# Kernel optimization log

Hardware: AMD Instinct MI355X
Metric: run time of the kernel (lower is better)

Reference implementation:

```python
import jax, jax.numpy as jnp
import numpy as np

BN_EPS = 1e-5


def three_nn(unknown, known):
    # unknown: (B,n,3), known: (B,m,3) -> dist (B,n,3), idx (B,n,3)
    d2 = (jnp.sum(unknown**2, -1)[:, :, None]
          + jnp.sum(known**2, -1)[:, None, :]
          - 2.0 * jnp.einsum('bnd,bmd->bnm', unknown, known))
    neg_d2, idx = jax.lax.top_k(-d2, 3)  # 3 smallest squared distances
    dist = jnp.sqrt(jnp.maximum(-neg_d2, 0.0))
    return dist, idx


def three_interpolate(points, idx, weight):
    # points: (B,m,c), idx: (B,n,3), weight: (B,n,3) -> (B,n,c)
    gathered = jax.vmap(lambda f, i: f[i])(points, idx)  # (B,n,3,c)
    return jnp.einsum('bnk,bnkc->bnc', weight, gathered)


def conv_bn_relu(x, W, b, g, beta):
    # 1x1 conv over points == per-point linear; BN over (batch, points)
    y = jnp.einsum('bnc,oc->bno', x, W) + b
    mu = jnp.mean(y, axis=(0, 1))
    var = jnp.var(y, axis=(0, 1))
    y = (y - mu) * jax.lax.rsqrt(var + BN_EPS) * g + beta
    return jax.nn.relu(y)


def setup_inputs() -> dict:
    key = jax.random.key(0)
    ks = jax.random.split(key, 8)
    B, n, m, C1, C2 = 8, 8192, 2048, 128, 256
    Cin = C1 + C2  # 384
    H = 256
    return {
        'unknown': jax.random.normal(ks[0], (B, n, 3), jnp.float32),
        'known': jax.random.normal(ks[1], (B, m, 3), jnp.float32),
        'unknow_feats': jax.random.normal(ks[2], (B, n, C1), jnp.float32),
        'known_feats': jax.random.normal(ks[3], (B, m, C2), jnp.float32),
        'W1': jax.random.normal(ks[4], (H, Cin), jnp.float32) * (1.0 / np.sqrt(Cin)),
        'b1': jnp.zeros((H,), jnp.float32),
        'g1': jnp.ones((H,), jnp.float32),
        'beta1': jnp.zeros((H,), jnp.float32),
        'W2': jax.random.normal(ks[5], (H, H), jnp.float32) * (1.0 / np.sqrt(H)),
        'b2': jnp.zeros((H,), jnp.float32),
        'g2': jnp.ones((H,), jnp.float32),
        'beta2': jnp.zeros((H,), jnp.float32),
    }


def reference(unknown, known, unknow_feats, known_feats,
              W1, b1, g1, beta1, W2, b2, g2, beta2):
    dist, idx = three_nn(unknown, known)
    dist = dist + 1e-10
    dist_recip = 1.0 / dist
    weight = dist_recip / jnp.sum(dist_recip, axis=2, keepdims=True)  # (B,n,3)
    interpolated = three_interpolate(known_feats, idx, weight)        # (B,n,C2)
    new_points = jnp.concatenate([interpolated, unknow_feats], axis=-1)  # (B,n,C1+C2)
    new_points = conv_bn_relu(new_points, W1, b1, g1, beta1)
    new_points = conv_bn_relu(new_points, W2, b2, g2, beta2)
    return new_points  # (B,n,mlp[-1])
```

## Files before the change

kernel.cpp:

```cpp
#include <hip/hip_runtime.h>

#define BQ   8
#define NQ   8192
#define MK   2048
#define C1v  128
#define C2v  256
#define CIN  384
#define HH   256
#define MTOT (BQ*NQ)

#define NCHUNK 8
#define CHSZ   (MK/NCHUNK)

typedef __attribute__((ext_vector_type(8))) __bf16 bf16x8;
typedef __attribute__((ext_vector_type(4))) float f32x4;
typedef __attribute__((ext_vector_type(8))) unsigned short us8;
typedef __attribute__((ext_vector_type(4))) unsigned short us4;
typedef __attribute__((ext_vector_type(2))) unsigned short us2;

__device__ __forceinline__ unsigned short f2bf(float f) {
  unsigned int u = __builtin_bit_cast(unsigned int, f);
  u += 0x7fffu + ((u >> 16) & 1u);
  return (unsigned short)(u >> 16);
}
__device__ __forceinline__ float bf2f(unsigned short h) {
  unsigned int u = ((unsigned int)h) << 16;
  return __builtin_bit_cast(float, u);
}

__device__ __forceinline__ void gload16(const void* g, void* l) {
  __builtin_amdgcn_global_load_lds((const __attribute__((address_space(1))) void*)g,
                                   (__attribute__((address_space(3))) void*)l, 16, 0, 0);
}

__device__ __forceinline__ unsigned int cvtpk_bf16(float lo, float hi) {
  unsigned int r;
  asm("v_cvt_pk_bf16_f32 %0, %1, %2" : "=v"(r) : "v"(lo), "v"(hi));
  return r;
}

#define SCORE(k4) (fmaf((k4).x, ux, fmaf((k4).y, uy, (k4).z * uz)) + (k4).w)

__device__ __forceinline__ double packsd(float s, int negj) {
  unsigned long long u = __builtin_bit_cast(unsigned long long, (double)s)
                       | (unsigned long long)(unsigned int)negj;
  return __builtin_bit_cast(double, u);
}

#define INS3D(s0, s1, s2, t)                                  \
  do {                                                        \
    double _hi0 = fmax(s0, (t)), _lo0 = fmin(s0, (t));        \
    double _hi1 = fmax(s1, _lo0), _lo1 = fmin(s1, _lo0);      \
    s0 = _hi0; s1 = _hi1; s2 = fmax(s2, _lo1);                \
  } while (0)

__global__ __launch_bounds__(256)
void prep_kernel(const float* __restrict__ W1, const float* __restrict__ W2,
                 const float* __restrict__ known,
                 unsigned short* __restrict__ w1b, unsigned short* __restrict__ w2b,
                 float* __restrict__ stats, float4* __restrict__ kprep) {
  int i = blockIdx.x * 256 + threadIdx.x;
  if (i < HH*CIN) w1b[i] = f2bf(W1[i]);
  else if (i < HH*CIN + HH*HH) w2b[i - HH*CIN] = f2bf(W2[i - HH*CIN]);
  int z = i - (HH*CIN + HH*HH);
  if (z >= 0 && z < 1024) stats[z] = 0.f;
  int z2 = i - (HH*CIN + HH*HH + 1024);
  if (z2 >= 0 && z2 < BQ*MK) {
    const float* kp = known + (size_t)z2 * 3;
    float x = kp[0], y = kp[1], zz = kp[2];
    kprep[z2] = make_float4(x, y, zz, -0.5f*(x*x + y*y + zz*zz));
  }
}

__global__ __launch_bounds__(512)
void nn_kernel(const float* __restrict__ unknown, const float4* __restrict__ kprep,
               int* __restrict__ widx, float* __restrict__ wwgt) {
  __shared__ double pd[NCHUNK][64][3];
  const int b = blockIdx.y;
  const int tid = threadIdx.x;
  const int wave = tid >> 6, lane = tid & 63;

  const int q = blockIdx.x * 64 + lane;
  const float* up = unknown + ((size_t)b * NQ + q) * 3;
  const float ux = up[0], uy = up[1], uz = up[2];
  const float nu = ux*ux + uy*uy + uz*uz;
  const int jbase = wave * CHSZ;
  const float4* cp = kprep + (b << 11) + __builtin_amdgcn_readfirstlane(jbase);

  double A0=-1e300, A1=-1e300, A2=-1e300;
  double B0=-1e300, B1=-1e300, B2=-1e300;
  #pragma unroll 4
  for (int j = 0; j < CHSZ; j += 2) {
    float4 ka = cp[j];
    float4 kc = cp[j+1];
    float sA = SCORE(ka);
    float sB = SCORE(kc);
    double da = packsd(sA, 2047 - (jbase + j));
    double db = packsd(sB, 2047 - (jbase + j + 1));
    INS3D(A0, A1, A2, da);
    INS3D(B0, B1, B2, db);
  }
  INS3D(A0, A1, A2, B0);
  INS3D(A0, A1, A2, B1);
  INS3D(A0, A1, A2, B2);
  pd[wave][lane][0] = A0; pd[wave][lane][1] = A1; pd[wave][lane][2] = A2;
  __syncthreads();

  if (tid < 64) {
    double f0=-1e300, f1=-1e300, f2=-1e300;
    #pragma unroll
    for (int c = 0; c < NCHUNK; ++c) {
      INS3D(f0, f1, f2, pd[c][tid][0]);
      INS3D(f0, f1, f2, pd[c][tid][1]);
      INS3D(f0, f1, f2, pd[c][tid][2]);
    }
    unsigned long long u0 = __builtin_bit_cast(unsigned long long, f0);
    unsigned long long u1 = __builtin_bit_cast(unsigned long long, f1);
    unsigned long long u2 = __builtin_bit_cast(unsigned long long, f2);
    int x0 = 2047 - (int)(u0 & 2047ULL);
    int x1 = 2047 - (int)(u1 & 2047ULL);
    int x2 = 2047 - (int)(u2 & 2047ULL);
    float s0 = (float)__builtin_bit_cast(double, u0 & ~2047ULL);
    float s1 = (float)__builtin_bit_cast(double, u1 & ~2047ULL);
    float s2 = (float)__builtin_bit_cast(double, u2 & ~2047ULL);
    float d0 = sqrtf(fmaxf(nu - 2.f*s0, 0.f)) + 1e-10f;
    float d1 = sqrtf(fmaxf(nu - 2.f*s1, 0.f)) + 1e-10f;
    float d2 = sqrtf(fmaxf(nu - 2.f*s2, 0.f)) + 1e-10f;
    float r0 = 1.f/d0, r1 = 1.f/d1, r2 = 1.f/d2;
    float rs = 1.f/(r0 + r1 + r2);
    size_t p = (size_t)b * NQ + q;
    widx[p*3+0] = x0;    widx[p*3+1] = x1;    widx[p*3+2] = x2;
    wwgt[p*3+0] = r0*rs; wwgt[p*3+1] = r1*rs; wwgt[p*3+2] = r2*rs;
  }
}

__global__ __launch_bounds__(256)
void gemm1_fused(const float* __restrict__ kf, const float* __restrict__ uf,
                 const int* __restrict__ widx, const float* __restrict__ wwgt,
                 const unsigned short* __restrict__ Bw,
                 const float* __restrict__ bias,
                 unsigned short* __restrict__ Out,
                 float* __restrict__ gsum, float* __restrict__ gsq) {
  constexpr int K = CIN;
  __shared__ unsigned short As[128][64];
  __shared__ unsigned short Bs[128][64];
  const int tid  = threadIdx.x;
  const int lane = tid & 63;
  const int wave = tid >> 6;
  const int wid   = blockIdx.x;
  const int batch = wid & 7;
  const int inner = wid >> 3;
  const int bm = batch * 64 + (inner >> 1);
  const int bn = inner & 1;
  const int wm = wave >> 1, wn = wave & 1;

  unsigned int vo0[4], vo1[4], vo2[4], voU[4];
  float w0r[4], w1r[4], w2r[4];
  #pragma unroll
  for (int i = 0; i < 4; ++i) {
    const int c = wave*64 + i*256 + lane;
    const int row = c >> 3, colB = (c & 7) * 32;
    const int p = bm*128 + row;
    const int b = p >> 13;
    w0r[i] = wwgt[p*3+0]; w1r[i] = wwgt[p*3+1]; w2r[i] = wwgt[p*3+2];
    vo0[i] = ((unsigned)((b << 11) + widx[p*3+0]) << 10) + colB;
    vo1[i] = ((unsigned)((b << 11) + widx[p*3+1]) << 10) + colB;
    vo2[i] = ((unsigned)((b << 11) + widx[p*3+2]) << 10) + colB;
    voU[i] = (unsigned)p * 512u + colB;
  }

  f32x4 acc[4][4];
  const f32x4 zero = {0.f, 0.f, 0.f, 0.f};
  #pragma unroll
  for (int m = 0; m < 4; ++m)
    #pragma unroll
    for (int n = 0; n < 4; ++n) acc[m][n] = zero;

  const char* kfb = (const char*)kf;
  const char* ufb = (const char*)uf;

  #pragma unroll
  for (int t = 0; t < 6; ++t) {
    const int k0 = t * 64;
    #pragma unroll
    for (int i = 0; i < 4; ++i) {
      const int cbase = wave*64 + i*256;
      const int c = cbase + lane;
      const int brow = c >> 3, bcol = (c & 7) * 8;
      gload16(Bw + ((size_t)(bn*128 + brow))*K + k0 + bcol, (unsigned short*)Bs + cbase*8);
      float4 r0, r1;
      if (t < 4) {
        float4 a0 = *(const float4*)(kfb + vo0[i] + k0*4);
        float4 a1 = *(const float4*)(kfb + vo0[i] + k0*4 + 16);
        float4 e0 = *(const float4*)(kfb + vo1[i] + k0*4);
        float4 e1 = *(const float4*)(kfb + vo1[i] + k0*4 + 16);
        float4 g0 = *(const float4*)(kfb + vo2[i] + k0*4);
        float4 g1 = *(const float4*)(kfb + vo2[i] + k0*4 + 16);
        const float w0 = w0r[i], w1 = w1r[i], w2 = w2r[i];
        r0.x = w0*a0.x + w1*e0.x + w2*g0.x;
        r0.y = w0*a0.y + w1*e0.y + w2*g0.y;
        r0.z = w0*a0.z + w1*e0.z + w2*g0.z;
        r0.w = w0*a0.w + w1*e0.w + w2*g0.w;
        r1.x = w0*a1.x + w1*e1.x + w2*g1.x;
        r1.y = w0*a1.y + w1*e1.y + w2*g1.y;
        r1.z = w0*a1.z + w1*e1.z + w2*g1.z;
        r1.w = w0*a1.w + w1*e1.w + w2*g1.w;
      } else {
        r0 = *(const float4*)(ufb + voU[i] + (k0 - 256)*4);
        r1 = *(const float4*)(ufb + voU[i] + (k0 - 256)*4 + 16);
      }
      uint4 ov;
      ov.x = cvtpk_bf16(r0.x, r0.y);
      ov.y = cvtpk_bf16(r0.z, r0.w);
      ov.z = cvtpk_bf16(r1.x, r1.y);
      ov.w = cvtpk_bf16(r1.z, r1.w);
      *(uint4*)((unsigned short*)As + (size_t)c*8) = ov;
    }
    __syncthreads();
    const int kq = (lane >> 4) * 8;
    #pragma unroll
    for (int kk = 0; kk < 64; kk += 32) {
      bf16x8 af[4], bfr[4];
      #pragma unroll
      for (int m = 0; m < 4; ++m)
        af[m] = *(const bf16x8*)&As[wm*64 + m*16 + (lane & 15)][kk + kq];
      #pragma unroll
      for (int n = 0; n < 4; ++n)
        bfr[n] = *(const bf16x8*)&Bs[wn*64 + n*16 + (lane & 15)][kk + kq];
      #pragma unroll
      for (int m = 0; m < 4; ++m)
        #pragma unroll
        for (int n = 0; n < 4; ++n)
          acc[m][n] = __builtin_amdgcn_mfma_f32_16x16x32_bf16(af[m], bfr[n], acc[m][n], 0, 0, 0);
    }
    __syncthreads();
  }

  float* s_sum = (float*)&As[0][0];
  float* s_sq  = s_sum + 256;
  #pragma unroll
  for (int n = 0; n < 4; ++n) {
    const int cb   = wn*64 + n*16 + (lane & 15);
    const int gcol = bn*128 + cb;
    const float bv = bias[gcol];
    float sum = 0.f, sq = 0.f;
    #pragma unroll
    for (int m = 0; m < 4; ++m) {
      const size_t grow = (size_t)bm*128 + wm*64 + m*16 + (lane >> 4)*4;
      #pragma unroll
      for (int qq = 0; qq < 4; ++qq) {
        float y = acc[m][n][qq] + bv;
        sum += y; sq += y*y;
        Out[(grow+qq)*256 + gcol] = f2bf(y);
      }
    }
    sum += __shfl_xor(sum, 16, 64); sum += __shfl_xor(sum, 32, 64);
    sq  += __shfl_xor(sq , 16, 64); sq  += __shfl_xor(sq , 32, 64);
    if (lane < 16) { s_sum[wm*128 + cb] = sum; s_sq[wm*128 + cb] = sq; }
  }
  __syncthreads();
  if (tid < 128) {
    atomicAdd(&gsum[bn*128 + tid], s_sum[tid] + s_sum[128 + tid]);
    atomicAdd(&gsq [bn*128 + tid], s_sq [tid] + s_sq [128 + tid]);
  }
}

__global__ __launch_bounds__(256)
void gemm2_kernel(const unsigned short* __restrict__ A,
                  const unsigned short* __restrict__ Bw,
                  const float* __restrict__ bias,
                  unsigned short* __restrict__ Out,
                  float* __restrict__ gsum, float* __restrict__ gsq,
                  const float* __restrict__ gsum1, const float* __restrict__ gsq1,
                  const float* __restrict__ g1, const float* __restrict__ be1) {
  constexpr int K = HH;
  __shared__ unsigned short As[128][64];
  __shared__ unsigned short Bs[128][64];
  __shared__ float sc_l[HH], sh_l[HH];
  const int tid  = threadIdx.x;
  const int lane = tid & 63;
  const int wave = tid >> 6;
  const int wid  = blockIdx.x;
  const int slot = wid & 15;
  const int bm = ((wid >> 4) << 3) | (slot & 7);
  const int bn = slot >> 3;
  const int wm = wave >> 1, wn = wave & 1;

  {
    float mu  = gsum1[tid] * (1.f/65536.f);
    float var = gsq1[tid]  * (1.f/65536.f) - mu*mu;
    float sc  = g1[tid] * rsqrtf(var + 1e-5f);
    sc_l[tid] = sc;
    sh_l[tid] = be1[tid] - mu*sc;
  }
  __syncthreads();

  f32x4 acc[4][4];
  const f32x4 zero = {0.f, 0.f, 0.f, 0.f};
  #pragma unroll
  for (int m = 0; m < 4; ++m)
    #pragma unroll
    for (int n = 0; n < 4; ++n) acc[m][n] = zero;

  for (int k0 = 0; k0 < K; k0 += 64) {
    #pragma unroll
    for (int i = 0; i < 4; ++i) {
      const int cbase = wave*64 + i*256;
      const int c = cbase + lane;
      const int row = c >> 3, col = (c & 7) * 8;
      gload16(Bw + ((size_t)(bn*128 + row))*K + k0 + col, (unsigned short*)Bs + cbase*8);
      us8 v = *(const us8*)(A + ((size_t)(bm*128 + row))*K + k0 + col);
      us8 o;
      #pragma unroll
      for (int j = 0; j < 8; ++j) {
        float y = fmaxf(fmaf(bf2f(v[j]), sc_l[k0+col+j], sh_l[k0+col+j]), 0.f);
        o[j] = f2bf(y);
      }
      *(us8*)((unsigned short*)As + cbase*8 + lane*8) = o;
    }
    __syncthreads();
    const int kq = (lane >> 4) * 8;
    #pragma unroll
    for (int kk = 0; kk < 64; kk += 32) {
      bf16x8 af[4], bfr[4];
      #pragma unroll
      for (int m = 0; m < 4; ++m)
        af[m] = *(const bf16x8*)&As[wm*64 + m*16 + (lane & 15)][kk + kq];
      #pragma unroll
      for (int n = 0; n < 4; ++n)
        bfr[n] = *(const bf16x8*)&Bs[wn*64 + n*16 + (lane & 15)][kk + kq];
      #pragma unroll
      for (int m = 0; m < 4; ++m)
        #pragma unroll
        for (int n = 0; n < 4; ++n)
          acc[m][n] = __builtin_amdgcn_mfma_f32_16x16x32_bf16(af[m], bfr[n], acc[m][n], 0, 0, 0);
    }
    __syncthreads();
  }

  float* s_sum = (float*)&As[0][0];
  float* s_sq  = s_sum + 256;
  #pragma unroll
  for (int n = 0; n < 4; ++n) {
    const int cb   = wn*64 + n*16 + (lane & 15);
    const int gcol = bn*128 + cb;
    const float bv = bias[gcol];
    float sum = 0.f, sq = 0.f;
    #pragma unroll
    for (int m = 0; m < 4; ++m) {
      const size_t grow = (size_t)bm*128 + wm*64 + m*16 + (lane >> 4)*4;
      #pragma unroll
      for (int qq = 0; qq < 4; ++qq) {
        float y = acc[m][n][qq] + bv;
        sum += y; sq += y*y;
        Out[(grow+qq)*256 + gcol] = f2bf(y);
      }
    }
    sum += __shfl_xor(sum, 16, 64); sum += __shfl_xor(sum, 32, 64);
    sq  += __shfl_xor(sq , 16, 64); sq  += __shfl_xor(sq , 32, 64);
    if (lane < 16) { s_sum[wm*128 + cb] = sum; s_sq[wm*128 + cb] = sq; }
  }
  __syncthreads();
  if (tid < 128) {
    atomicAdd(&gsum[bn*128 + tid], s_sum[tid] + s_sum[128 + tid]);
    atomicAdd(&gsq [bn*128 + tid], s_sq [tid] + s_sq [128 + tid]);
  }
}

__global__ __launch_bounds__(256)
void final_kernel(const unsigned short* __restrict__ Y2, float* __restrict__ Out,
                  const float* __restrict__ gsum, const float* __restrict__ gsq,
                  const float* __restrict__ g2, const float* __restrict__ be2) {
  __shared__ float sc[256], sh[256];
  {
    float mu  = gsum[threadIdx.x] * (1.f/65536.f);
    float var = gsq[threadIdx.x]  * (1.f/65536.f) - mu*mu;
    float scv = g2[threadIdx.x] * rsqrtf(var + 1e-5f);
    sc[threadIdx.x] = scv;
    sh[threadIdx.x] = be2[threadIdx.x] - mu*scv;
  }
  __syncthreads();
  size_t i = ((size_t)blockIdx.x * 256 + threadIdx.x) * 8;
  int c0 = (int)(i & 255);
  us8 v = *(const us8*)(Y2 + i);
  float4 o1, o2;
  o1.x = fmaxf(fmaf(bf2f(v[0]), sc[c0+0], sh[c0+0]), 0.f);
  o1.y = fmaxf(fmaf(bf2f(v[1]), sc[c0+1], sh[c0+1]), 0.f);
  o1.z = fmaxf(fmaf(bf2f(v[2]), sc[c0+2], sh[c0+2]), 0.f);
  o1.w = fmaxf(fmaf(bf2f(v[3]), sc[c0+3], sh[c0+3]), 0.f);
  o2.x = fmaxf(fmaf(bf2f(v[4]), sc[c0+4], sh[c0+4]), 0.f);
  o2.y = fmaxf(fmaf(bf2f(v[5]), sc[c0+5], sh[c0+5]), 0.f);
  o2.z = fmaxf(fmaf(bf2f(v[6]), sc[c0+6], sh[c0+6]), 0.f);
  o2.w = fmaxf(fmaf(bf2f(v[7]), sc[c0+7], sh[c0+7]), 0.f);
  *(float4*)(Out + i)     = o1;
  *(float4*)(Out + i + 4) = o2;
}

extern "C" void kernel_launch(void* const* d_in, const int* in_sizes, int n_in,
                              void* d_out, int out_size, void* d_ws, size_t ws_size,
                              hipStream_t stream) {
  const float* unknown = (const float*)d_in[0];
  const float* known   = (const float*)d_in[1];
  const float* uf      = (const float*)d_in[2];
  const float* kf      = (const float*)d_in[3];
  const float* W1      = (const float*)d_in[4];
  const float* b1      = (const float*)d_in[5];
  const float* g1      = (const float*)d_in[6];
  const float* be1     = (const float*)d_in[7];
  const float* W2      = (const float*)d_in[8];
  const float* b2      = (const float*)d_in[9];
  const float* g2      = (const float*)d_in[10];
  const float* be2     = (const float*)d_in[11];

  char* ws = (char*)d_ws;
  unsigned short* X    = (unsigned short*)(ws);
  unsigned short* Y1   = (unsigned short*)(ws + 50331648);
  unsigned short* w1b  = (unsigned short*)(ws + 83886080);
  unsigned short* w2b  = (unsigned short*)(ws + 84082688);
  int*            widx = (int*)  (ws + 84213760);
  float*          wwgt = (float*)(ws + 85000192);
  float*          stats= (float*)(ws + 85786624);
  float4*         kprep= (float4*)(ws + 85794816);
  float *sum1 = stats,        *sq1 = stats + 256;
  float *sum2 = stats + 512,  *sq2 = stats + 768;
  float* out = (float*)d_out;

  prep_kernel<<<708, 256, 0, stream>>>(W1, W2, known, w1b, w2b, stats, kprep);
  nn_kernel<<<dim3(128, 8), 512, 0, stream>>>(unknown, kprep, widx, wwgt);
  gemm1_fused<<<1024, 256, 0, stream>>>(kf, uf, widx, wwgt, w1b, b1, Y1, sum1, sq1);
  gemm2_kernel<<<1024, 256, 0, stream>>>(Y1, w2b, b2, X, sum2, sq2, sum1, sq1, g1, be1);
  final_kernel<<<8192, 256, 0, stream>>>(X, out, sum2, sq2, g2, be2);
}
```

Baseline: 159.9 us.

## Pre-convert known features to bf16 and software-pipeline gathers in gemm1

Adds a pass in the prep kernel that converts known_feats to bf16 into the X workspace buffer. gemm1 then gathers half as many bytes per neighbour. The gathers for the next K-tile are issued into double-buffered registers before the current tile is converted and stored, so global load latency overlaps with the LDS writes and MFMA work. The costs are an extra conversion pass over a 16 MB tensor, higher register pressure from the prefetch buffers, and bf16 rounding of the features before interpolation.

Result: faster. 146.8 us (-8.3%).

```diff
diff --git a/kernel.cpp b/kernel.cpp
--- a/kernel.cpp
+++ b/kernel.cpp
@@ -56,9 +56,10 @@
 
 __global__ __launch_bounds__(256)
 void prep_kernel(const float* __restrict__ W1, const float* __restrict__ W2,
-                 const float* __restrict__ known,
+                 const float* __restrict__ known, const float* __restrict__ kf,
                  unsigned short* __restrict__ w1b, unsigned short* __restrict__ w2b,
-                 float* __restrict__ stats, float4* __restrict__ kprep) {
+                 float* __restrict__ stats, float4* __restrict__ kprep,
+                 unsigned short* __restrict__ kfb) {
   int i = blockIdx.x * 256 + threadIdx.x;
   if (i < HH*CIN) w1b[i] = f2bf(W1[i]);
   else if (i < HH*CIN + HH*HH) w2b[i - HH*CIN] = f2bf(W2[i - HH*CIN]);
@@ -69,6 +70,15 @@
     const float* kp = known + (size_t)z2 * 3;
     float x = kp[0], y = kp[1], zz = kp[2];
     kprep[z2] = make_float4(x, y, zz, -0.5f*(x*x + y*y + zz*zz));
+  }
+  int z3 = i - (HH*CIN + HH*HH + 1024 + BQ*MK);
+  if (z3 >= 0 && z3 < (BQ*MK*C2v)/8) {
+    const float4* src = (const float4*)(kf + (size_t)z3 * 8);
+    float4 v0 = src[0], v1 = src[1];
+    us8 o;
+    o[0]=f2bf(v0.x); o[1]=f2bf(v0.y); o[2]=f2bf(v0.z); o[3]=f2bf(v0.w);
+    o[4]=f2bf(v1.x); o[5]=f2bf(v1.y); o[6]=f2bf(v1.z); o[7]=f2bf(v1.w);
+    *(us8*)(kfb + (size_t)z3 * 8) = o;
   }
 }
 
@@ -135,7 +145,7 @@
 }
 
 __global__ __launch_bounds__(256)
-void gemm1_fused(const float* __restrict__ kf, const float* __restrict__ uf,
+void gemm1_fused(const unsigned short* __restrict__ kfb, const float* __restrict__ uf,
                  const int* __restrict__ widx, const float* __restrict__ wwgt,
                  const unsigned short* __restrict__ Bw,
                  const float* __restrict__ bias,
@@ -154,19 +164,21 @@
   const int bn = inner & 1;
   const int wm = wave >> 1, wn = wave & 1;
 
-  unsigned int vo0[4], vo1[4], vo2[4], voU[4];
+  unsigned int voK0[4], voK1[4], voK2[4], voU[4];
   float w0r[4], w1r[4], w2r[4];
   #pragma unroll
   for (int i = 0; i < 4; ++i) {
     const int c = wave*64 + i*256 + lane;
-    const int row = c >> 3, colB = (c & 7) * 32;
+    const int row = c >> 3;
+    const int colK = (c & 7) * 16;
+    const int colU = (c & 7) * 32;
     const int p = bm*128 + row;
     const int b = p >> 13;
     w0r[i] = wwgt[p*3+0]; w1r[i] = wwgt[p*3+1]; w2r[i] = wwgt[p*3+2];
-    vo0[i] = ((unsigned)((b << 11) + widx[p*3+0]) << 10) + colB;
-    vo1[i] = ((unsigned)((b << 11) + widx[p*3+1]) << 10) + colB;
-    vo2[i] = ((unsigned)((b << 11) + widx[p*3+2]) << 10) + colB;
-    voU[i] = (unsigned)p * 512u + colB;
+    voK0[i] = ((unsigned)((b << 11) + widx[p*3+0]) << 9) + colK;
+    voK1[i] = ((unsigned)((b << 11) + widx[p*3+1]) << 9) + colK;
+    voK2[i] = ((unsigned)((b << 11) + widx[p*3+2]) << 9) + colK;
+    voU[i]  = (unsigned)p * 512u + colU;
   }
 
   f32x4 acc[4][4];
@@ -176,11 +188,22 @@
     #pragma unroll
     for (int n = 0; n < 4; ++n) acc[m][n] = zero;
 
-  const char* kfb = (const char*)kf;
-  const char* ufb = (const char*)uf;
+  const char* kfbb = (const char*)kfb;
+  const char* ufb  = (const char*)uf;
+
+  us8    PK0[2][4], PK1[2][4], PK2[2][4];
+  float4 PU0[2][4], PU1[2][4];
+
+  #pragma unroll
+  for (int i = 0; i < 4; ++i) {
+    PK0[0][i] = *(const us8*)(kfbb + voK0[i]);
+    PK1[0][i] = *(const us8*)(kfbb + voK1[i]);
+    PK2[0][i] = *(const us8*)(kfbb + voK2[i]);
+  }
 
   #pragma unroll
   for (int t = 0; t < 6; ++t) {
+    const int cur = t & 1, nxt = cur ^ 1;
     const int k0 = t * 64;
     #pragma unroll
     for (int i = 0; i < 4; ++i) {
@@ -188,32 +211,47 @@
       const int c = cbase + lane;
       const int brow = c >> 3, bcol = (c & 7) * 8;
       gload16(Bw + ((size_t)(bn*128 + brow))*K + k0 + bcol, (unsigned short*)Bs + cbase*8);
-      float4 r0, r1;
+    }
+    if (t < 3) {
+      #pragma unroll
+      for (int i = 0; i < 4; ++i) {
+        PK0[nxt][i] = *(const us8*)(kfbb + voK0[i] + (t+1)*128);
+        PK1[nxt][i] = *(const us8*)(kfbb + voK1[i] + (t+1)*128);
+        PK2[nxt][i] = *(const us8*)(kfbb + voK2[i] + (t+1)*128);
+      }
+    } else if (t < 5) {
+      #pragma unroll
+      for (int i = 0; i < 4; ++i) {
+        PU0[nxt][i] = *(const float4*)(ufb + voU[i] + (t-3)*256);
+        PU1[nxt][i] = *(const float4*)(ufb + voU[i] + (t-3)*256 + 16);
+      }
+    }
+    __builtin_amdgcn_sched_barrier(0);
+    #pragma unroll
+    for (int i = 0; i < 4; ++i) {
+      const int c = wave*64 + i*256 + lane;
+      uint4 ov;
       if (t < 4) {
-        float4 a0 = *(const float4*)(kfb + vo0[i] + k0*4);
-        float4 a1 = *(const float4*)(kfb + vo0[i] + k0*4 + 16);
-        float4 e0 = *(const float4*)(kfb + vo1[i] + k0*4);
-        float4 e1 = *(const float4*)(kfb + vo1[i] + k0*4 + 16);
-        float4 g0 = *(const float4*)(kfb + vo2[i] + k0*4);
-        float4 g1 = *(const float4*)(kfb + vo2[i] + k0*4 + 16);
         const float w0 = w0r[i], w1 = w1r[i], w2 = w2r[i];
-        r0.x = w0*a0.x + w1*e0.x + w2*g0.x;
-        r0.y = w0*a0.y + w1*e0.y + w2*g0.y;
-        r0.z = w0*a0.z + w1*e0.z + w2*g0.z;
-        r0.w = w0*a0.w + w1*e0.w + w2*g0.w;
-        r1.x = w0*a1.x + w1*e1.x + w2*g1.x;
-        r1.y = w0*a1.y + w1*e1.y + w2*g1.y;
-        r1.z = w0*a1.z + w1*e1.z + w2*g1.z;
-        r1.w = w0*a1.w + w1*e1.w + w2*g1.w;
+        float r[8];
+        #pragma unroll
+        for (int j = 0; j < 8; ++j) {
+          float fa = bf2f((unsigned short)PK0[cur][i][j]);
+          float fe = bf2f((unsigned short)PK1[cur][i][j]);
+          float fg = bf2f((unsigned short)PK2[cur][i][j]);
+          r[j] = w0*fa + w1*fe + w2*fg;
+        }
+        ov.x = cvtpk_bf16(r[0], r[1]);
+        ov.y = cvtpk_bf16(r[2], r[3]);
+        ov.z = cvtpk_bf16(r[4], r[5]);
+        ov.w = cvtpk_bf16(r[6], r[7]);
       } else {
-        r0 = *(const float4*)(ufb + voU[i] + (k0 - 256)*4);
-        r1 = *(const float4*)(ufb + voU[i] + (k0 - 256)*4 + 16);
-      }
-      uint4 ov;
-      ov.x = cvtpk_bf16(r0.x, r0.y);
-      ov.y = cvtpk_bf16(r0.z, r0.w);
-      ov.z = cvtpk_bf16(r1.x, r1.y);
-      ov.w = cvtpk_bf16(r1.z, r1.w);
+        float4 r0 = PU0[cur][i], r1 = PU1[cur][i];
+        ov.x = cvtpk_bf16(r0.x, r0.y);
+        ov.y = cvtpk_bf16(r0.z, r0.w);
+        ov.z = cvtpk_bf16(r1.x, r1.y);
+        ov.w = cvtpk_bf16(r1.z, r1.w);
+      }
       *(uint4*)((unsigned short*)As + (size_t)c*8) = ov;
     }
     __syncthreads();
@@ -425,9 +463,9 @@
   float *sum2 = stats + 512,  *sq2 = stats + 768;
   float* out = (float*)d_out;
 
-  prep_kernel<<<708, 256, 0, stream>>>(W1, W2, known, w1b, w2b, stats, kprep);
+  prep_kernel<<<2757, 256, 0, stream>>>(W1, W2, known, kf, w1b, w2b, stats, kprep, X);
   nn_kernel<<<dim3(128, 8), 512, 0, stream>>>(unknown, kprep, widx, wwgt);
-  gemm1_fused<<<1024, 256, 0, stream>>>(kf, uf, widx, wwgt, w1b, b1, Y1, sum1, sq1);
+  gemm1_fused<<<1024, 256, 0, stream>>>(X, uf, widx, wwgt, w1b, b1, Y1, sum1, sq1);
   gemm2_kernel<<<1024, 256, 0, stream>>>(Y1, w2b, b2, X, sum2, sq2, sum1, sq1, g1, be1);
   final_kernel<<<8192, 256, 0, stream>>>(X, out, sum2, sq2, g2, be2);
 }
```
